# Optimization experiments

Hardware: AMD Instinct MI355X
Metric: run time of the kernel (lower is better)

## Reference

```python
import jax, jax.numpy as jnp
import numpy as np

EPS = 1e-6
NUM_STAGES = 7
NUM_FILTERS = 8


def _gaussian_kernel(size=5, sigma=1.0):
    ax = np.arange(size) - (size - 1) / 2.0
    g = np.exp(-(ax ** 2) / (2.0 * sigma ** 2))
    k = np.outer(g, g)
    k = k / k.sum()
    return jnp.asarray(k, dtype=jnp.float32).reshape(1, 1, size, size)


def _refl_conv(x, k, p):
    # reflect-pad then VALID correlation (matches F.pad(mode='reflect') + F.conv2d)
    xp = jnp.pad(x, ((0, 0), (0, 0), (p, p), (p, p)), mode='reflect')
    return jax.lax.conv_general_dilated(xp, k, (1, 1), 'VALID',
                                        dimension_numbers=('NCHW', 'OIHW', 'NCHW'))


def setup_inputs() -> dict:
    key = jax.random.key(0)
    k1, k2, k3, k4 = jax.random.split(key, 4)
    B, H, W = 8, 512, 512
    noisy = jax.random.uniform(k1, (B, 1, H, W), dtype=jnp.float32, minval=0.05, maxval=1.0)
    # per-stage fixed analysis filters (buffer in torch): randn / sqrt(k*k)
    filters = jax.random.normal(k2, (NUM_STAGES, NUM_FILTERS, 1, 3, 3), dtype=jnp.float32) / 3.0
    # depthwise 1x1 influence projection: weight + bias per channel per stage
    w = jax.random.normal(k3, (NUM_STAGES, NUM_FILTERS), dtype=jnp.float32)
    b = jax.random.normal(k4, (NUM_STAGES, NUM_FILTERS), dtype=jnp.float32) * 0.1
    lam = jnp.full((NUM_STAGES,), 0.1, dtype=jnp.float32)
    gate = jnp.full((NUM_STAGES,), -2.0, dtype=jnp.float32)
    gauss = _gaussian_kernel(5, 1.0)
    return {"noisy": noisy, "filters": filters, "w": w, "b": b,
            "lam": lam, "gate": gate, "gauss": gauss, "looks": 4}


def reference(noisy, filters, w, b, lam, gate, gauss, looks):
    del looks  # unused when use_level_embedding=False
    est = noisy  # initial_estimate is identity
    for s in range(filters.shape[0]):
        f = filters[s]  # [C,1,3,3]
        # u_sigma: 5x5 gaussian smoothing with reflect padding
        u_sigma = _refl_conv(est, gauss, 2)
        iw = jnp.maximum(
            u_sigma / jnp.maximum(jnp.max(u_sigma, axis=(2, 3), keepdims=True), EPS),
            EPS)  # [B,1,H,W]
        # analysis conv: 1 -> C channels
        resp = _refl_conv(est, f, 1)  # [B,C,H,W]
        # depthwise 1x1 conv + tanh influence
        infl = jnp.tanh(resp * w[s][None, :, None, None] + b[s][None, :, None, None])
        z = iw * infl
        # conv_transpose2d(z, flip(f), padding=1) == conv2d(z, f^T as (1,C,3,3), zero pad 1)
        diff = jax.lax.conv_general_dilated(
            z, jnp.transpose(f, (1, 0, 2, 3)), (1, 1), ((1, 1), (1, 1)),
            dimension_numbers=('NCHW', 'OIHW', 'NCHW'))  # [B,1,H,W]
        fidelity_grad = (est - noisy) / (est * est + EPS)
        est2 = est - diff - lam[s] * iw * fidelity_grad
        g = jax.nn.sigmoid(gate[s])
        est = jnp.clip(est2 + g * (noisy - est2), EPS, 1.0)
    return jnp.clip(est, EPS, 1.0)
```

## Files before the change

kernel.cpp:

```cpp
#include <hip/hip_runtime.h>
#include <hip/hip_bf16.h>

#define EPS 1e-6f
#define H 512
#define W 512
#define NB 8
#define NC 8
#define NS 7
#define LOG2E 1.4426950408889634f

typedef float v2f __attribute__((ext_vector_type(2)));

__device__ __forceinline__ int refl(int t, int n) {
    if (t < 0) t = -t;
    if (t >= n) t = 2 * n - 2 - t;
    return t;
}

#define GW 256
#define GR 8
#define NBLK ((W / GW) * (H / GR))

__global__ __launch_bounds__(256) void gauss_max_kernel(
    const float* __restrict__ est, const float* __restrict__ gauss,
    float* __restrict__ blockmax)
{
    const int tx = threadIdx.x, ty = threadIdx.y;
    const int x0 = blockIdx.x * GW;
    const int R  = blockIdx.y * GR + ty * 2;
    const int b  = blockIdx.z;
    const float* e = est + (size_t)b * H * W;
    const int c0 = x0 + tx * 4;

    const float g0 = sqrtf(gauss[0]);
    const float g1 = sqrtf(gauss[6]);
    const float g2 = sqrtf(gauss[12]);

    float4 h0, h1, h2, h3, h4;
    float m = 0.f;

#pragma unroll
    for (int k = 0; k < 6; k++) {
        const float* row = e + refl(R - 2 + k, H) * W;
        float4 v = *(const float4*)&row[c0];
        float em2 = __shfl_up(v.z, 1);
        float em1 = __shfl_up(v.w, 1);
        float ep1 = __shfl_down(v.x, 1);
        float ep2 = __shfl_down(v.y, 1);
        if (tx == 0) {
            if (x0 == 0) { em2 = v.z; em1 = v.y; }
            else         { em2 = row[c0 - 2]; em1 = row[c0 - 1]; }
        }
        if (tx == 63) {
            if (x0 + GW == W) { ep1 = v.z; ep2 = v.y; }
            else              { ep1 = row[c0 + 4]; ep2 = row[c0 + 5]; }
        }
        float4 hc;
        hc.x = g0 * (em2 + v.z) + g1 * (em1 + v.y) + g2 * v.x;
        hc.y = g0 * (em1 + v.w) + g1 * (v.x + v.z) + g2 * v.y;
        hc.z = g0 * (v.x + ep1) + g1 * (v.y + v.w) + g2 * v.z;
        hc.w = g0 * (v.y + ep2) + g1 * (v.z + ep1) + g2 * v.w;
        h0 = h1; h1 = h2; h2 = h3; h3 = h4; h4 = hc;
        if (k >= 4) {
            float ux = g0 * (h0.x + h4.x) + g1 * (h1.x + h3.x) + g2 * h2.x;
            float uy = g0 * (h0.y + h4.y) + g1 * (h1.y + h3.y) + g2 * h2.y;
            float uz = g0 * (h0.z + h4.z) + g1 * (h1.z + h3.z) + g2 * h2.z;
            float uw = g0 * (h0.w + h4.w) + g1 * (h1.w + h3.w) + g2 * h2.w;
            m = fmaxf(m, fmaxf(fmaxf(ux, uy), fmaxf(uz, uw)));
        }
    }

#pragma unroll
    for (int off = 32; off > 0; off >>= 1)
        m = fmaxf(m, __shfl_xor(m, off, 64));
    __shared__ float wm[4];
    if (tx == 0) wm[ty] = m;
    __syncthreads();
    if (tx == 0 && ty == 0) {
        float mm = fmaxf(fmaxf(wm[0], wm[1]), fmaxf(wm[2], wm[3]));
        blockmax[b * NBLK + blockIdx.y * gridDim.x + blockIdx.x] = mm;
    }
}

#define SLAB 8
#define BANDW 58
#define NBANDS 9

__global__ __launch_bounds__(64) void stage_kernel(
    const float* __restrict__ est, const float* __restrict__ noisy,
    const float* __restrict__ blockmax,
    const float* __restrict__ filt,
    const float* __restrict__ wv, const float* __restrict__ bv,
    const float* __restrict__ lamp, const float* __restrict__ gatep,
    const float* __restrict__ gauss,
    float* __restrict__ out)
{
    const int l = threadIdx.x;
    const int band = blockIdx.x;
    const int R = blockIdx.y * SLAB;
    const int b = blockIdx.z;

    const float* e  = est   + (size_t)b * H * W;
    const float* nz = noisy + (size_t)b * H * W;
    float*       op = out   + (size_t)b * H * W;

    const int c = band * BANDW - 3 + l;
    const int ci0 = refl(c - 2, W), ci1 = refl(c - 1, W), ci2 = refl(c, W),
              ci3 = refl(c + 1, W), ci4 = refl(c + 2, W);
    const int cc = c < 0 ? 0 : (c > W - 1 ? W - 1 : c);
    const bool c_in = (c >= 0) && (c < W);
    const bool c_st = (l >= 3) && (l <= 60) && (c < W);

    v2f fp[9][4], w2p[4], b2p[4];
#pragma unroll
    for (int j = 0; j < 4; j++) {
#pragma unroll
        for (int k = 0; k < 9; k++)
            fp[k][j] = (v2f){filt[(2 * j) * 9 + k], filt[(2 * j + 1) * 9 + k]};
        w2p[j] = (v2f){wv[2 * j] * (2.f * LOG2E), wv[2 * j + 1] * (2.f * LOG2E)};
        b2p[j] = (v2f){bv[2 * j] * (2.f * LOG2E), bv[2 * j + 1] * (2.f * LOG2E)};
    }

    const float g0 = sqrtf(gauss[0]);
    const float g1 = sqrtf(gauss[6]);
    const float g2 = sqrtf(gauss[12]);
    const float lam = lamp[0];
    const float g = __builtin_amdgcn_rcpf(1.f + __builtin_amdgcn_exp2f(-gatep[0] * LOG2E));

    float m = fmaxf(blockmax[b * NBLK + l], blockmax[b * NBLK + 64 + l]);
#pragma unroll
    for (int off = 32; off > 0; off >>= 1)
        m = fmaxf(m, __shfl_xor(m, off, 64));
    const float dinv = __builtin_amdgcn_rcpf(fmaxf(m, EPS));

    auto ld5 = [&](int r, float& m2, float& m1, float& v, float& p1, float& p2) {
        const float* rb = e + (size_t)refl(r, H) * W;
        m2 = rb[ci0]; m1 = rb[ci1]; v = rb[ci2]; p1 = rb[ci3]; p2 = rb[ci4];
    };
    auto hof = [&](float m2, float m1, float v, float p1, float p2) -> float {
        return g0 * (m2 + p2) + g1 * (m1 + p1) + g2 * v;
    };
    auto ldn = [&](int r) -> float {
        int rr = r < 0 ? 0 : (r > H - 1 ? H - 1 : r);
        return nz[(size_t)rr * W + cc];
    };

    float h[5];
    float wm1[4], wvv[4], wp1[4];
    {
        float m2, m1, v, p1, p2;
        ld5(R - 3, m2, m1, v, p1, p2); h[1] = hof(m2, m1, v, p1, p2);
        ld5(R - 2, m2, m1, v, p1, p2); h[2] = hof(m2, m1, v, p1, p2);
        wm1[1] = m1; wvv[1] = v; wp1[1] = p1;
        ld5(R - 1, m2, m1, v, p1, p2); h[3] = hof(m2, m1, v, p1, p2);
        wm1[2] = m1; wvv[2] = v; wp1[2] = p1;
        ld5(R - 0, m2, m1, v, p1, p2); h[4] = hof(m2, m1, v, p1, p2);
        wm1[3] = m1; wvv[3] = v; wp1[3] = p1;
    }
    float qm2[3], qm1[3], qv[3], qp1[3], qp2[3];
    ld5(R + 1, qm2[0], qm1[0], qv[0], qp1[0], qp2[0]);
    ld5(R + 2, qm2[1], qm1[1], qv[1], qp1[1], qp2[1]);
    ld5(R + 3, qm2[2], qm1[2], qv[2], qp1[2], qp2[2]);
    float nq0 = ldn(R - 2), nq1 = ldn(R - 1), nq2 = ldn(R);
    wm1[0] = 0.f; wvv[0] = 0.f; wp1[0] = 0.f; h[0] = 0.f;

    v2f aU0 = {0,0}, aV0 = {0,0}, aW0 = {0,0};
    v2f aU1 = {0,0}, aV1 = {0,0}, aW1 = {0,0};
    float iw_prev = 0.f;

#pragma unroll 2
    for (int i = 0; i < SLAB + 2; ++i) {
        const int t = R - 1 + i;

        float m2 = qm2[0], m1 = qm1[0], v = qv[0], p1 = qp1[0], p2 = qp2[0];
        qm2[0] = qm2[1]; qm1[0] = qm1[1]; qv[0] = qv[1]; qp1[0] = qp1[1]; qp2[0] = qp2[1];
        qm2[1] = qm2[2]; qm1[1] = qm1[2]; qv[1] = qv[2]; qp1[1] = qp1[2]; qp2[1] = qp2[2];
        ld5(t + 5, qm2[2], qm1[2], qv[2], qp1[2], qp2[2]);
        float n0 = nq0; nq0 = nq1; nq1 = nq2; nq2 = ldn(t + 2);

        float hnew = hof(m2, m1, v, p1, p2);
        h[0] = h[1]; h[1] = h[2]; h[2] = h[3]; h[3] = h[4]; h[4] = hnew;
        float iw = fmaxf((g0 * (h[0] + h[4]) + g1 * (h[1] + h[3]) + g2 * h[2]) * dinv, EPS);
        const bool rin = (t >= 0) && (t < H);
        if (!(c_in && rin)) iw = 0.f;

        wm1[0] = wm1[1]; wvv[0] = wvv[1]; wp1[0] = wp1[1];
        wm1[1] = wm1[2]; wvv[1] = wvv[2]; wp1[1] = wp1[2];
        wm1[2] = wm1[3]; wvv[2] = wvv[3]; wp1[2] = wp1[3];
        wm1[3] = m1;     wvv[3] = v;      wp1[3] = p1;

        float ew[9] = {wm1[0], wvv[0], wp1[0],
                       wm1[1], wvv[1], wp1[1],
                       wm1[2], wvv[2], wp1[2]};
        v2f r4[4] = {{0,0},{0,0},{0,0},{0,0}};
#pragma unroll
        for (int k = 0; k < 9; k++) {
            v2f es = (v2f){ew[k], ew[k]};
            r4[0] += fp[k][0] * es;
            r4[1] += fp[k][1] * es;
            r4[2] += fp[k][2] * es;
            r4[3] += fp[k][3] * es;
        }
        v2f zp[4];
        v2f iwv = (v2f){iw, iw};
#pragma unroll
        for (int j = 0; j < 4; j++) {
            v2f wr = w2p[j] * r4[j] + b2p[j];
            float a0 = __builtin_amdgcn_exp2f(wr.x);
            float a1 = __builtin_amdgcn_exp2f(wr.y);
            v2f th = (v2f){1.f - 2.f * __builtin_amdgcn_rcpf(a0 + 1.f),
                           1.f - 2.f * __builtin_amdgcn_rcpf(a1 + 1.f)};
            zp[j] = iwv * th;
        }
        v2f U0 = {0,0}, V0 = {0,0}, W0 = {0,0};
        v2f U1 = {0,0}, V1 = {0,0}, W1 = {0,0};
        v2f U2 = {0,0}, V2 = {0,0}, W2 = {0,0};
#pragma unroll
        for (int j = 0; j < 4; j++) {
            U0 += fp[0][j] * zp[j]; V0 += fp[1][j] * zp[j]; W0 += fp[2][j] * zp[j];
            U1 += fp[3][j] * zp[j]; V1 += fp[4][j] * zp[j]; W1 += fp[5][j] * zp[j];
            U2 += fp[6][j] * zp[j]; V2 += fp[7][j] * zp[j]; W2 += fp[8][j] * zp[j];
        }
        v2f dU = aU0 + U2, dV = aV0 + V2, dW = aW0 + W2;
        aU0 = aU1 + U1; aV0 = aV1 + V1; aW0 = aW1 + W1;
        aU1 = U0;       aV1 = V0;       aW1 = W0;
        float dUs = dU.x + dU.y, dVs = dV.x + dV.y, dWs = dW.x + dW.y;
        float diff = __shfl_up(dUs, 1) + dVs + __shfl_down(dWs, 1);

        if (i >= 2 && c_st) {
            float eo = wvv[0];
            float fg = (eo - n0) * __builtin_amdgcn_rcpf(eo * eo + EPS);
            float est2 = eo - diff - lam * iw_prev * fg;
            float en = est2 + g * (n0 - est2);
            en = fminf(fmaxf(en, EPS), 1.f);
            op[(size_t)(t - 1) * W + c] = en;
        }
        iw_prev = iw;
    }
}

extern "C" void kernel_launch(void* const* d_in, const int* in_sizes, int n_in,
                              void* d_out, int out_size, void* d_ws, size_t ws_size,
                              hipStream_t stream)
{
    const float* noisy   = (const float*)d_in[0];
    const float* filters = (const float*)d_in[1];
    const float* wv      = (const float*)d_in[2];
    const float* bv      = (const float*)d_in[3];
    const float* lam     = (const float*)d_in[4];
    const float* gate    = (const float*)d_in[5];
    const float* gauss   = (const float*)d_in[6];
    float* out = (float*)d_out;

    char* ws = (char*)d_ws;
    float* ws0      = (float*)ws;
    float* blockmax = (float*)(ws + (8u << 20));

    const float* cur = noisy;
    for (int s = 0; s < NS; s++) {
        float* nxt = (s % 2 == 0) ? out : ws0;
        gauss_max_kernel<<<dim3(W / GW, H / GR, NB), dim3(64, 4), 0, stream>>>(
            cur, gauss, blockmax);
        stage_kernel<<<dim3(NBANDS, H / SLAB, NB), dim3(64), 0, stream>>>(
            cur, noisy, blockmax,
            filters + s * NC * 9, wv + s * NC, bv + s * NC, lam + s, gate + s, gauss, nxt);
        cur = nxt;
    }
}
```

Measured before the change: 266.0 us.

## Process two adjacent columns per lane with float2 loads in stage kernel

Each lane of the stage kernel now computes two neighbouring output columns instead of one. Bands grow from 58 to 124 outputs, with 5 bands instead of 9. Row loads become three float2 loads per row rather than five scalar loads, and reflect padding at the image edges is handled with select fixups. The intent is to cut redundant halo loads and recomputation across bands and to vectorize global loads and stores. In exchange each lane carries roughly twice the register state, and the row loop is now fully unrolled.

```diff
diff --git a/kernel.cpp b/kernel.cpp
--- a/kernel.cpp
+++ b/kernel.cpp
@@ -83,8 +83,8 @@
 }
 
 #define SLAB 8
-#define BANDW 58
-#define NBANDS 9
+#define OUTB 124
+#define NBANDS 5
 
 __global__ __launch_bounds__(64) void stage_kernel(
     const float* __restrict__ est, const float* __restrict__ noisy,
@@ -104,12 +104,15 @@
     const float* nz = noisy + (size_t)b * H * W;
     float*       op = out   + (size_t)b * H * W;
 
-    const int c = band * BANDW - 3 + l;
-    const int ci0 = refl(c - 2, W), ci1 = refl(c - 1, W), ci2 = refl(c, W),
-              ci3 = refl(c + 1, W), ci4 = refl(c + 2, W);
-    const int cc = c < 0 ? 0 : (c > W - 1 ? W - 1 : c);
-    const bool c_in = (c >= 0) && (c < W);
-    const bool c_st = (l >= 3) && (l <= 60) && (c < W);
+    const int c0 = OUTB * band - 2 + 2 * l;
+    const int a0 = min(max(c0 - 2, 0), W - 2);
+    const int a1 = min(max(c0,     0), W - 2);
+    const int a2 = min(max(c0 + 2, 0), W - 2);
+    const bool fixL = (c0 == 0);
+    const bool fixR = (c0 == W - 2);
+    const bool rvin0 = (c0 >= 0) && (c0 < W);
+    const bool rvin1 = (c0 + 1 >= 0) && (c0 + 1 < W);
+    const bool do_store = (l >= 1) && (l <= 62) && (c0 >= 0) && (c0 <= W - 2);
 
     v2f fp[9][4], w2p[4], b2p[4];
 #pragma unroll
@@ -133,109 +136,154 @@
         m = fmaxf(m, __shfl_xor(m, off, 64));
     const float dinv = __builtin_amdgcn_rcpf(fmaxf(m, EPS));
 
-    auto ld5 = [&](int r, float& m2, float& m1, float& v, float& p1, float& p2) {
+    auto ld3 = [&](int r, v2f& Lv, v2f& Mv, v2f& Rv) {
         const float* rb = e + (size_t)refl(r, H) * W;
-        m2 = rb[ci0]; m1 = rb[ci1]; v = rb[ci2]; p1 = rb[ci3]; p2 = rb[ci4];
+        Lv = *(const v2f*)&rb[a0];
+        Mv = *(const v2f*)&rb[a1];
+        Rv = *(const v2f*)&rb[a2];
     };
-    auto hof = [&](float m2, float m1, float v, float p1, float p2) -> float {
-        return g0 * (m2 + p2) + g1 * (m1 + p1) + g2 * v;
+    auto ldn = [&](int r) -> v2f {
+        int rr = min(max(r, 0), H - 1);
+        return *(const v2f*)&nz[(size_t)rr * W + a1];
     };
-    auto ldn = [&](int r) -> float {
-        int rr = r < 0 ? 0 : (r > H - 1 ? H - 1 : r);
-        return nz[(size_t)rr * W + cc];
+    auto taps = [&](v2f Lv, v2f Mv, v2f Rv, float& m2, float& m1,
+                    float& v0, float& v1, float& p1, float& p2) {
+        v0 = Mv.x; v1 = Mv.y;
+        m2 = fixL ? Rv.x : Lv.x;
+        m1 = fixL ? Mv.y : Lv.y;
+        p1 = fixR ? Mv.x : Rv.x;
+        p2 = fixR ? Lv.y : Rv.y;
     };
-
-    float h[5];
-    float wm1[4], wvv[4], wp1[4];
+    auto hof = [&](float m2, float m1, float v0, float v1, float p1, float p2) -> v2f {
+        return (v2f){ g0 * (m2 + p1) + g1 * (m1 + v1) + g2 * v0,
+                      g0 * (m1 + p2) + g1 * (v0 + p1) + g2 * v1 };
+    };
+
+    v2f h[5];
+    float wm1[4], wv0[4], wv1[4], wp1[4];
+
     {
-        float m2, m1, v, p1, p2;
-        ld5(R - 3, m2, m1, v, p1, p2); h[1] = hof(m2, m1, v, p1, p2);
-        ld5(R - 2, m2, m1, v, p1, p2); h[2] = hof(m2, m1, v, p1, p2);
-        wm1[1] = m1; wvv[1] = v; wp1[1] = p1;
-        ld5(R - 1, m2, m1, v, p1, p2); h[3] = hof(m2, m1, v, p1, p2);
-        wm1[2] = m1; wvv[2] = v; wp1[2] = p1;
-        ld5(R - 0, m2, m1, v, p1, p2); h[4] = hof(m2, m1, v, p1, p2);
-        wm1[3] = m1; wvv[3] = v; wp1[3] = p1;
-    }
-    float qm2[3], qm1[3], qv[3], qp1[3], qp2[3];
-    ld5(R + 1, qm2[0], qm1[0], qv[0], qp1[0], qp2[0]);
-    ld5(R + 2, qm2[1], qm1[1], qv[1], qp1[1], qp2[1]);
-    ld5(R + 3, qm2[2], qm1[2], qv[2], qp1[2], qp2[2]);
-    float nq0 = ldn(R - 2), nq1 = ldn(R - 1), nq2 = ldn(R);
-    wm1[0] = 0.f; wvv[0] = 0.f; wp1[0] = 0.f; h[0] = 0.f;
+        v2f Lv, Mv, Rv; float m2, m1, v0, v1, p1, p2;
+        ld3(R - 3, Lv, Mv, Rv); taps(Lv, Mv, Rv, m2, m1, v0, v1, p1, p2);
+        h[1] = hof(m2, m1, v0, v1, p1, p2);
+        ld3(R - 2, Lv, Mv, Rv); taps(Lv, Mv, Rv, m2, m1, v0, v1, p1, p2);
+        h[2] = hof(m2, m1, v0, v1, p1, p2);
+        wm1[1] = m1; wv0[1] = v0; wv1[1] = v1; wp1[1] = p1;
+        ld3(R - 1, Lv, Mv, Rv); taps(Lv, Mv, Rv, m2, m1, v0, v1, p1, p2);
+        h[3] = hof(m2, m1, v0, v1, p1, p2);
+        wm1[2] = m1; wv0[2] = v0; wv1[2] = v1; wp1[2] = p1;
+        ld3(R - 0, Lv, Mv, Rv); taps(Lv, Mv, Rv, m2, m1, v0, v1, p1, p2);
+        h[4] = hof(m2, m1, v0, v1, p1, p2);
+        wm1[3] = m1; wv0[3] = v0; wv1[3] = v1; wp1[3] = p1;
+    }
+    h[0] = (v2f){0.f, 0.f};
+    wm1[0] = 0.f; wv0[0] = 0.f; wv1[0] = 0.f; wp1[0] = 0.f;
+
+    v2f qL[3], qM[3], qR[3], qn[3];
+    ld3(R + 1, qL[0], qM[0], qR[0]);
+    ld3(R + 2, qL[1], qM[1], qR[1]);
+    ld3(R + 3, qL[2], qM[2], qR[2]);
+    qn[0] = ldn(R - 2); qn[1] = ldn(R - 1); qn[2] = ldn(R);
 
     v2f aU0 = {0,0}, aV0 = {0,0}, aW0 = {0,0};
     v2f aU1 = {0,0}, aV1 = {0,0}, aW1 = {0,0};
-    float iw_prev = 0.f;
-
-#pragma unroll 2
+    v2f iw_prev = {0,0};
+
+#pragma unroll
     for (int i = 0; i < SLAB + 2; ++i) {
         const int t = R - 1 + i;
 
-        float m2 = qm2[0], m1 = qm1[0], v = qv[0], p1 = qp1[0], p2 = qp2[0];
-        qm2[0] = qm2[1]; qm1[0] = qm1[1]; qv[0] = qv[1]; qp1[0] = qp1[1]; qp2[0] = qp2[1];
-        qm2[1] = qm2[2]; qm1[1] = qm1[2]; qv[1] = qv[2]; qp1[1] = qp1[2]; qp2[1] = qp2[2];
-        ld5(t + 5, qm2[2], qm1[2], qv[2], qp1[2], qp2[2]);
-        float n0 = nq0; nq0 = nq1; nq1 = nq2; nq2 = ldn(t + 2);
-
-        float hnew = hof(m2, m1, v, p1, p2);
-        h[0] = h[1]; h[1] = h[2]; h[2] = h[3]; h[3] = h[4]; h[4] = hnew;
-        float iw = fmaxf((g0 * (h[0] + h[4]) + g1 * (h[1] + h[3]) + g2 * h[2]) * dinv, EPS);
+        v2f Lc = qL[0], Mc = qM[0], Rc = qR[0];
+        qL[0] = qL[1]; qL[1] = qL[2];
+        qM[0] = qM[1]; qM[1] = qM[2];
+        qR[0] = qR[1]; qR[1] = qR[2];
+        ld3(t + 5, qL[2], qM[2], qR[2]);
+        v2f nv = qn[0]; qn[0] = qn[1]; qn[1] = qn[2]; qn[2] = ldn(t + 2);
+
+        float m2, m1, v0, v1, p1, p2;
+        taps(Lc, Mc, Rc, m2, m1, v0, v1, p1, p2);
+        v2f hn = hof(m2, m1, v0, v1, p1, p2);
+        h[0] = h[1]; h[1] = h[2]; h[2] = h[3]; h[3] = h[4]; h[4] = hn;
+
+        v2f iwv = g0 * (h[0] + h[4]) + g1 * (h[1] + h[3]) + g2 * h[2];
         const bool rin = (t >= 0) && (t < H);
-        if (!(c_in && rin)) iw = 0.f;
-
-        wm1[0] = wm1[1]; wvv[0] = wvv[1]; wp1[0] = wp1[1];
-        wm1[1] = wm1[2]; wvv[1] = wvv[2]; wp1[1] = wp1[2];
-        wm1[2] = wm1[3]; wvv[2] = wvv[3]; wp1[2] = wp1[3];
-        wm1[3] = m1;     wvv[3] = v;      wp1[3] = p1;
-
-        float ew[9] = {wm1[0], wvv[0], wp1[0],
-                       wm1[1], wvv[1], wp1[1],
-                       wm1[2], wvv[2], wp1[2]};
-        v2f r4[4] = {{0,0},{0,0},{0,0},{0,0}};
-#pragma unroll
-        for (int k = 0; k < 9; k++) {
-            v2f es = (v2f){ew[k], ew[k]};
-            r4[0] += fp[k][0] * es;
-            r4[1] += fp[k][1] * es;
-            r4[2] += fp[k][2] * es;
-            r4[3] += fp[k][3] * es;
-        }
-        v2f zp[4];
-        v2f iwv = (v2f){iw, iw};
+        float iwa = (rvin0 && rin) ? fmaxf(iwv.x * dinv, EPS) : 0.f;
+        float iwb = (rvin1 && rin) ? fmaxf(iwv.y * dinv, EPS) : 0.f;
+
+        wm1[0] = wm1[1]; wv0[0] = wv0[1]; wv1[0] = wv1[1]; wp1[0] = wp1[1];
+        wm1[1] = wm1[2]; wv0[1] = wv0[2]; wv1[1] = wv1[2]; wp1[1] = wp1[2];
+        wm1[2] = wm1[3]; wv0[2] = wv0[3]; wv1[2] = wv1[3]; wp1[2] = wp1[3];
+        wm1[3] = m1;     wv0[3] = v0;     wv1[3] = v1;     wp1[3] = p1;
+
+        v2f ra[4] = {{0,0},{0,0},{0,0},{0,0}};
+        v2f rb[4] = {{0,0},{0,0},{0,0},{0,0}};
+#pragma unroll
+        for (int row = 0; row < 3; row++) {
+            const float ta[4] = {wm1[row], wv0[row], wv1[row], wp1[row]};
+#pragma unroll
+            for (int dx = 0; dx < 3; dx++) {
+                const int k = row * 3 + dx;
+                v2f ea2 = (v2f){ta[dx], ta[dx]};
+                v2f eb2 = (v2f){ta[dx + 1], ta[dx + 1]};
+#pragma unroll
+                for (int j = 0; j < 4; j++) {
+                    ra[j] += fp[k][j] * ea2;
+                    rb[j] += fp[k][j] * eb2;
+                }
+            }
+        }
+        v2f zpa[4], zpb[4];
+        const v2f iwa2 = (v2f){iwa, iwa}, iwb2 = (v2f){iwb, iwb};
 #pragma unroll
         for (int j = 0; j < 4; j++) {
-            v2f wr = w2p[j] * r4[j] + b2p[j];
-            float a0 = __builtin_amdgcn_exp2f(wr.x);
-            float a1 = __builtin_amdgcn_exp2f(wr.y);
-            v2f th = (v2f){1.f - 2.f * __builtin_amdgcn_rcpf(a0 + 1.f),
-                           1.f - 2.f * __builtin_amdgcn_rcpf(a1 + 1.f)};
-            zp[j] = iwv * th;
-        }
-        v2f U0 = {0,0}, V0 = {0,0}, W0 = {0,0};
-        v2f U1 = {0,0}, V1 = {0,0}, W1 = {0,0};
-        v2f U2 = {0,0}, V2 = {0,0}, W2 = {0,0};
-#pragma unroll
-        for (int j = 0; j < 4; j++) {
-            U0 += fp[0][j] * zp[j]; V0 += fp[1][j] * zp[j]; W0 += fp[2][j] * zp[j];
-            U1 += fp[3][j] * zp[j]; V1 += fp[4][j] * zp[j]; W1 += fp[5][j] * zp[j];
-            U2 += fp[6][j] * zp[j]; V2 += fp[7][j] * zp[j]; W2 += fp[8][j] * zp[j];
-        }
-        v2f dU = aU0 + U2, dV = aV0 + V2, dW = aW0 + W2;
-        aU0 = aU1 + U1; aV0 = aV1 + V1; aW0 = aW1 + W1;
-        aU1 = U0;       aV1 = V0;       aW1 = W0;
-        float dUs = dU.x + dU.y, dVs = dV.x + dV.y, dWs = dW.x + dW.y;
-        float diff = __shfl_up(dUs, 1) + dVs + __shfl_down(dWs, 1);
-
-        if (i >= 2 && c_st) {
-            float eo = wvv[0];
-            float fg = (eo - n0) * __builtin_amdgcn_rcpf(eo * eo + EPS);
-            float est2 = eo - diff - lam * iw_prev * fg;
-            float en = est2 + g * (n0 - est2);
-            en = fminf(fmaxf(en, EPS), 1.f);
-            op[(size_t)(t - 1) * W + c] = en;
-        }
-        iw_prev = iw;
+            v2f wra = w2p[j] * ra[j] + b2p[j];
+            v2f wrb = w2p[j] * rb[j] + b2p[j];
+            v2f tha = (v2f){1.f - 2.f * __builtin_amdgcn_rcpf(__builtin_amdgcn_exp2f(wra.x) + 1.f),
+                            1.f - 2.f * __builtin_amdgcn_rcpf(__builtin_amdgcn_exp2f(wra.y) + 1.f)};
+            v2f thb = (v2f){1.f - 2.f * __builtin_amdgcn_rcpf(__builtin_amdgcn_exp2f(wrb.x) + 1.f),
+                            1.f - 2.f * __builtin_amdgcn_rcpf(__builtin_amdgcn_exp2f(wrb.y) + 1.f)};
+            zpa[j] = iwa2 * tha;
+            zpb[j] = iwb2 * thb;
+        }
+        v2f sa[9] = {{0,0},{0,0},{0,0},{0,0},{0,0},{0,0},{0,0},{0,0},{0,0}};
+        v2f sb[9] = {{0,0},{0,0},{0,0},{0,0},{0,0},{0,0},{0,0},{0,0},{0,0}};
+#pragma unroll
+        for (int j = 0; j < 4; j++)
+#pragma unroll
+            for (int k = 0; k < 9; k++) {
+                sa[k] += fp[k][j] * zpa[j];
+                sb[k] += fp[k][j] * zpb[j];
+            }
+        v2f U0v = (v2f){sa[0].x + sa[0].y, sb[0].x + sb[0].y};
+        v2f V0v = (v2f){sa[1].x + sa[1].y, sb[1].x + sb[1].y};
+        v2f W0v = (v2f){sa[2].x + sa[2].y, sb[2].x + sb[2].y};
+        v2f U1v = (v2f){sa[3].x + sa[3].y, sb[3].x + sb[3].y};
+        v2f V1v = (v2f){sa[4].x + sa[4].y, sb[4].x + sb[4].y};
+        v2f W1v = (v2f){sa[5].x + sa[5].y, sb[5].x + sb[5].y};
+        v2f U2v = (v2f){sa[6].x + sa[6].y, sb[6].x + sb[6].y};
+        v2f V2v = (v2f){sa[7].x + sa[7].y, sb[7].x + sb[7].y};
+        v2f W2v = (v2f){sa[8].x + sa[8].y, sb[8].x + sb[8].y};
+
+        v2f dU = aU0 + U2v, dV = aV0 + V2v, dW = aW0 + W2v;
+        aU0 = aU1 + U1v; aV0 = aV1 + V1v; aW0 = aW1 + W1v;
+        aU1 = U0v;       aV1 = V0v;       aW1 = W0v;
+
+        float difa = __shfl_up(dU.y, 1) + dV.x + dW.y;
+        float difb = dU.x + dV.y + __shfl_down(dW.x, 1);
+
+        if (i >= 2 && do_store) {
+            float eoa = wv0[0], eob = wv1[0];
+            float fga = (eoa - nv.x) * __builtin_amdgcn_rcpf(eoa * eoa + EPS);
+            float fgb = (eob - nv.y) * __builtin_amdgcn_rcpf(eob * eob + EPS);
+            float e2a = eoa - difa - lam * iw_prev.x * fga;
+            float e2b = eob - difb - lam * iw_prev.y * fgb;
+            float ena = e2a + g * (nv.x - e2a);
+            float enb = e2b + g * (nv.y - e2b);
+            ena = fminf(fmaxf(ena, EPS), 1.f);
+            enb = fminf(fmaxf(enb, EPS), 1.f);
+            *(v2f*)&op[(size_t)(t - 1) * W + c0] = (v2f){ena, enb};
+        }
+        iw_prev = (v2f){iwa, iwb};
     }
 }
 
```

Measured after the change: 280.9 us. 5.6% more time.

## Process two rows per iteration and double slab height in stage kernel

Applied to the files above, without the earlier changes.

Doubles the per-block row slab and restructures the streaming loop so each iteration computes two output rows, using explicit scalar registers instead of shifting arrays and pre-reducing the transposed-conv partials to scalars. The taller slab amortizes the halo rows (gaussian and 3x3 borders) over more outputs, halving grid size in the row dimension. Risks include higher register pressure, fewer blocks for occupancy, and a non-unrolled loop with more live values.

```diff
diff --git a/kernel.cpp b/kernel.cpp
--- a/kernel.cpp
+++ b/kernel.cpp
@@ -82,7 +82,7 @@
     }
 }
 
-#define SLAB 8
+#define SLAB 16
 #define BANDW 58
 #define NBANDS 9
 
@@ -145,97 +145,116 @@
         return nz[(size_t)rr * W + cc];
     };
 
-    float h[5];
-    float wm1[4], wvv[4], wp1[4];
+    float hA, hB, hC, hD;
+    float wm1_0, wv0_0, wp1_0, wm1_1, wv0_1, wp1_1, wm1_2, wv0_2, wp1_2;
     {
         float m2, m1, v, p1, p2;
-        ld5(R - 3, m2, m1, v, p1, p2); h[1] = hof(m2, m1, v, p1, p2);
-        ld5(R - 2, m2, m1, v, p1, p2); h[2] = hof(m2, m1, v, p1, p2);
-        wm1[1] = m1; wvv[1] = v; wp1[1] = p1;
-        ld5(R - 1, m2, m1, v, p1, p2); h[3] = hof(m2, m1, v, p1, p2);
-        wm1[2] = m1; wvv[2] = v; wp1[2] = p1;
-        ld5(R - 0, m2, m1, v, p1, p2); h[4] = hof(m2, m1, v, p1, p2);
-        wm1[3] = m1; wvv[3] = v; wp1[3] = p1;
-    }
-    float qm2[3], qm1[3], qv[3], qp1[3], qp2[3];
-    ld5(R + 1, qm2[0], qm1[0], qv[0], qp1[0], qp2[0]);
-    ld5(R + 2, qm2[1], qm1[1], qv[1], qp1[1], qp2[1]);
-    ld5(R + 3, qm2[2], qm1[2], qv[2], qp1[2], qp2[2]);
-    float nq0 = ldn(R - 2), nq1 = ldn(R - 1), nq2 = ldn(R);
-    wm1[0] = 0.f; wvv[0] = 0.f; wp1[0] = 0.f; h[0] = 0.f;
-
-    v2f aU0 = {0,0}, aV0 = {0,0}, aW0 = {0,0};
-    v2f aU1 = {0,0}, aV1 = {0,0}, aW1 = {0,0};
-    float iw_prev = 0.f;
-
-#pragma unroll 2
-    for (int i = 0; i < SLAB + 2; ++i) {
-        const int t = R - 1 + i;
-
-        float m2 = qm2[0], m1 = qm1[0], v = qv[0], p1 = qp1[0], p2 = qp2[0];
-        qm2[0] = qm2[1]; qm1[0] = qm1[1]; qv[0] = qv[1]; qp1[0] = qp1[1]; qp2[0] = qp2[1];
-        qm2[1] = qm2[2]; qm1[1] = qm1[2]; qv[1] = qv[2]; qp1[1] = qp1[2]; qp2[1] = qp2[2];
-        ld5(t + 5, qm2[2], qm1[2], qv[2], qp1[2], qp2[2]);
-        float n0 = nq0; nq0 = nq1; nq1 = nq2; nq2 = ldn(t + 2);
-
-        float hnew = hof(m2, m1, v, p1, p2);
-        h[0] = h[1]; h[1] = h[2]; h[2] = h[3]; h[3] = h[4]; h[4] = hnew;
-        float iw = fmaxf((g0 * (h[0] + h[4]) + g1 * (h[1] + h[3]) + g2 * h[2]) * dinv, EPS);
-        const bool rin = (t >= 0) && (t < H);
-        if (!(c_in && rin)) iw = 0.f;
-
-        wm1[0] = wm1[1]; wvv[0] = wvv[1]; wp1[0] = wp1[1];
-        wm1[1] = wm1[2]; wvv[1] = wvv[2]; wp1[1] = wp1[2];
-        wm1[2] = wm1[3]; wvv[2] = wvv[3]; wp1[2] = wp1[3];
-        wm1[3] = m1;     wvv[3] = v;      wp1[3] = p1;
-
-        float ew[9] = {wm1[0], wvv[0], wp1[0],
-                       wm1[1], wvv[1], wp1[1],
-                       wm1[2], wvv[2], wp1[2]};
-        v2f r4[4] = {{0,0},{0,0},{0,0},{0,0}};
+        ld5(R - 3, m2, m1, v, p1, p2); hA = hof(m2, m1, v, p1, p2);
+        ld5(R - 2, m2, m1, v, p1, p2); hB = hof(m2, m1, v, p1, p2);
+        wm1_0 = m1; wv0_0 = v; wp1_0 = p1;
+        ld5(R - 1, m2, m1, v, p1, p2); hC = hof(m2, m1, v, p1, p2);
+        wm1_1 = m1; wv0_1 = v; wp1_1 = p1;
+        ld5(R - 0, m2, m1, v, p1, p2); hD = hof(m2, m1, v, p1, p2);
+        wm1_2 = m1; wv0_2 = v; wp1_2 = p1;
+    }
+    float q0m2, q0m1, q0v, q0p1, q0p2;
+    float q1m2, q1m1, q1v, q1p1, q1p2;
+    float q2m2, q2m1, q2v, q2p1, q2p2;
+    float q3m2, q3m1, q3v, q3p1, q3p2;
+    ld5(R + 1, q0m2, q0m1, q0v, q0p1, q0p2);
+    ld5(R + 2, q1m2, q1m1, q1v, q1p1, q1p2);
+    ld5(R + 3, q2m2, q2m1, q2v, q2p1, q2p2);
+    ld5(R + 4, q3m2, q3m1, q3v, q3p1, q3p2);
+    float nq0 = ldn(R - 2), nq1 = ldn(R - 1), nq2 = ldn(R), nq3 = ldn(R + 1);
+
+    float aU0 = 0.f, aV0 = 0.f, aW0 = 0.f;
+    float aU1 = 0.f, aV1 = 0.f, aW1 = 0.f;
+    float iwp = 0.f;
+
+#pragma unroll 1
+    for (int i = 0; i < SLAB / 2 + 1; ++i) {
+        const int t = R - 1 + 2 * i;
+
+        float e2m2 = q0m2, e2m1 = q0m1, e2v = q0v, e2p1 = q0p1, e2p2 = q0p2;
+        float e3m2 = q1m2, e3m1 = q1m1, e3v = q1v, e3p1 = q1p1, e3p2 = q1p2;
+        q0m2 = q2m2; q0m1 = q2m1; q0v = q2v; q0p1 = q2p1; q0p2 = q2p2;
+        q1m2 = q3m2; q1m1 = q3m1; q1v = q3v; q1p1 = q3p1; q1p2 = q3p2;
+        ld5(t + 6, q2m2, q2m1, q2v, q2p1, q2p2);
+        ld5(t + 7, q3m2, q3m1, q3v, q3p1, q3p2);
+        float n0 = nq0, n1 = nq1;
+        nq0 = nq2; nq1 = nq3; nq2 = ldn(t + 3); nq3 = ldn(t + 4);
+
+        float h4 = hof(e2m2, e2m1, e2v, e2p1, e2p2);
+        float h5 = hof(e3m2, e3m1, e3v, e3p1, e3p2);
+        float iw_t  = fmaxf((g0 * (hA + h4) + g1 * (hB + hD) + g2 * hC) * dinv, EPS);
+        float iw_t1 = fmaxf((g0 * (hB + h5) + g1 * (hC + h4) + g2 * hD) * dinv, EPS);
+        if (!(c_in && t >= 0 && t < H))         iw_t  = 0.f;
+        if (!(c_in && t + 1 >= 0 && t + 1 < H)) iw_t1 = 0.f;
+        hA = hC; hB = hD; hC = h4; hD = h5;
+
+        const float taA[9] = {wm1_0, wv0_0, wp1_0, wm1_1, wv0_1, wp1_1, wm1_2, wv0_2, wp1_2};
+        const float taB[9] = {wm1_1, wv0_1, wp1_1, wm1_2, wv0_2, wp1_2, e2m1, e2v, e2p1};
+        v2f ra[4] = {{0,0},{0,0},{0,0},{0,0}};
+        v2f rb[4] = {{0,0},{0,0},{0,0},{0,0}};
 #pragma unroll
         for (int k = 0; k < 9; k++) {
-            v2f es = (v2f){ew[k], ew[k]};
-            r4[0] += fp[k][0] * es;
-            r4[1] += fp[k][1] * es;
-            r4[2] += fp[k][2] * es;
-            r4[3] += fp[k][3] * es;
-        }
-        v2f zp[4];
-        v2f iwv = (v2f){iw, iw};
+            v2f ea = (v2f){taA[k], taA[k]};
+            v2f eb = (v2f){taB[k], taB[k]};
+#pragma unroll
+            for (int j = 0; j < 4; j++) {
+                ra[j] += fp[k][j] * ea;
+                rb[j] += fp[k][j] * eb;
+            }
+        }
+        v2f zpa[4], zpb[4];
+        const v2f iwa2 = (v2f){iw_t, iw_t}, iwb2 = (v2f){iw_t1, iw_t1};
 #pragma unroll
         for (int j = 0; j < 4; j++) {
-            v2f wr = w2p[j] * r4[j] + b2p[j];
-            float a0 = __builtin_amdgcn_exp2f(wr.x);
-            float a1 = __builtin_amdgcn_exp2f(wr.y);
-            v2f th = (v2f){1.f - 2.f * __builtin_amdgcn_rcpf(a0 + 1.f),
-                           1.f - 2.f * __builtin_amdgcn_rcpf(a1 + 1.f)};
-            zp[j] = iwv * th;
-        }
-        v2f U0 = {0,0}, V0 = {0,0}, W0 = {0,0};
-        v2f U1 = {0,0}, V1 = {0,0}, W1 = {0,0};
-        v2f U2 = {0,0}, V2 = {0,0}, W2 = {0,0};
-#pragma unroll
-        for (int j = 0; j < 4; j++) {
-            U0 += fp[0][j] * zp[j]; V0 += fp[1][j] * zp[j]; W0 += fp[2][j] * zp[j];
-            U1 += fp[3][j] * zp[j]; V1 += fp[4][j] * zp[j]; W1 += fp[5][j] * zp[j];
-            U2 += fp[6][j] * zp[j]; V2 += fp[7][j] * zp[j]; W2 += fp[8][j] * zp[j];
-        }
-        v2f dU = aU0 + U2, dV = aV0 + V2, dW = aW0 + W2;
-        aU0 = aU1 + U1; aV0 = aV1 + V1; aW0 = aW1 + W1;
-        aU1 = U0;       aV1 = V0;       aW1 = W0;
-        float dUs = dU.x + dU.y, dVs = dV.x + dV.y, dWs = dW.x + dW.y;
-        float diff = __shfl_up(dUs, 1) + dVs + __shfl_down(dWs, 1);
-
-        if (i >= 2 && c_st) {
-            float eo = wvv[0];
-            float fg = (eo - n0) * __builtin_amdgcn_rcpf(eo * eo + EPS);
-            float est2 = eo - diff - lam * iw_prev * fg;
-            float en = est2 + g * (n0 - est2);
-            en = fminf(fmaxf(en, EPS), 1.f);
-            op[(size_t)(t - 1) * W + c] = en;
-        }
-        iw_prev = iw;
+            v2f wra = w2p[j] * ra[j] + b2p[j];
+            v2f wrb = w2p[j] * rb[j] + b2p[j];
+            v2f tha = (v2f){1.f - 2.f * __builtin_amdgcn_rcpf(__builtin_amdgcn_exp2f(wra.x) + 1.f),
+                            1.f - 2.f * __builtin_amdgcn_rcpf(__builtin_amdgcn_exp2f(wra.y) + 1.f)};
+            v2f thb = (v2f){1.f - 2.f * __builtin_amdgcn_rcpf(__builtin_amdgcn_exp2f(wrb.x) + 1.f),
+                            1.f - 2.f * __builtin_amdgcn_rcpf(__builtin_amdgcn_exp2f(wrb.y) + 1.f)};
+            zpa[j] = iwa2 * tha;
+            zpb[j] = iwb2 * thb;
+        }
+        float qa[9], qb[9];
+#pragma unroll
+        for (int k = 0; k < 9; k++) {
+            v2f sA = fp[k][0] * zpa[0] + fp[k][1] * zpa[1]
+                   + fp[k][2] * zpa[2] + fp[k][3] * zpa[3];
+            v2f sB = fp[k][0] * zpb[0] + fp[k][1] * zpb[1]
+                   + fp[k][2] * zpb[2] + fp[k][3] * zpb[3];
+            qa[k] = sA.x + sA.y;
+            qb[k] = sB.x + sB.y;
+        }
+        float dAU = aU0 + qa[6], dAV = aV0 + qa[7], dAW = aW0 + qa[8];
+        float dBU = aU1 + qa[3] + qb[6], dBV = aV1 + qa[4] + qb[7], dBW = aW1 + qa[5] + qb[8];
+        aU0 = qa[0] + qb[3]; aV0 = qa[1] + qb[4]; aW0 = qa[2] + qb[5];
+        aU1 = qb[0];         aV1 = qb[1];         aW1 = qb[2];
+        float diffA = __shfl_up(dAU, 1) + dAV + __shfl_down(dAW, 1);
+        float diffB = __shfl_up(dBU, 1) + dBV + __shfl_down(dBW, 1);
+
+        if (i >= 1 && c_st) {
+            float eoa = wv0_0;
+            float fga = (eoa - n0) * __builtin_amdgcn_rcpf(eoa * eoa + EPS);
+            float e2a = eoa - diffA - lam * iwp * fga;
+            float ena = e2a + g * (n0 - e2a);
+            ena = fminf(fmaxf(ena, EPS), 1.f);
+            op[(size_t)(t - 1) * W + c] = ena;
+            float eob = wv0_1;
+            float fgb = (eob - n1) * __builtin_amdgcn_rcpf(eob * eob + EPS);
+            float e2b = eob - diffB - lam * iw_t * fgb;
+            float enb = e2b + g * (n1 - e2b);
+            enb = fminf(fmaxf(enb, EPS), 1.f);
+            op[(size_t)t * W + c] = enb;
+        }
+        iwp = iw_t1;
+
+        wm1_0 = wm1_2; wv0_0 = wv0_2; wp1_0 = wp1_2;
+        wm1_1 = e2m1;  wv0_1 = e2v;   wp1_1 = e2p1;
+        wm1_2 = e3m1;  wv0_2 = e3v;   wp1_2 = e3p1;
     }
 }
 
```

New measurement: 282.7 us. +6.3%, slower.
